# Kernel tuning notes

Hardware: AMD Instinct MI355X
Metric: run time of the kernel (lower is better)

The kernel has to match this reference:

```python
import jax, jax.numpy as jnp
import numpy as np

INPUT_SIZE = 128
HIDDEN = 256
EPS = 1e-5  # PyTorch BatchNorm1d default


def setup_inputs() -> dict:
    key = jax.random.key(0)
    k1, k2, k3 = jax.random.split(key, 3)
    B, S = 128, 1024
    x = jax.random.normal(k1, (B, S, INPUT_SIZE), dtype=jnp.float32)
    fan_in = INPUT_SIZE + HIDDEN
    bound = 1.0 / np.sqrt(fan_in)
    # Linear(input+hidden -> 4*hidden); stored transposed for x @ W
    W = jax.random.uniform(k2, (fan_in, 4 * HIDDEN), minval=-bound, maxval=bound, dtype=jnp.float32)
    b = jax.random.uniform(k3, (4 * HIDDEN,), minval=-bound, maxval=bound, dtype=jnp.float32)
    gamma = jnp.ones((4, HIDDEN), dtype=jnp.float32)   # per-gate BN weight
    beta = jnp.zeros((4, HIDDEN), dtype=jnp.float32)   # per-gate BN bias
    return {"x": x, "W": W, "b": b, "gamma": gamma, "beta": beta}


def reference(x, W, b, gamma, beta):
    B, S, _ = x.shape
    H = HIDDEN

    def step(carry, x_t):
        hx, cx = carry
        g = jnp.concatenate([x_t, hx], axis=1) @ W + b          # [B, 4H]
        g = g.reshape(B, 4, H)
        # BatchNorm1d (training mode): batch statistics per gate/feature
        mean = g.mean(axis=0)                                   # [4, H]
        var = jnp.mean((g - mean) ** 2, axis=0)                 # biased var
        gn = (g - mean) * jax.lax.rsqrt(var + EPS) * gamma + beta
        i = jax.nn.sigmoid(gn[:, 0])
        f = jax.nn.sigmoid(gn[:, 1])
        c = jnp.tanh(gn[:, 2])
        o = jax.nn.sigmoid(gn[:, 3])
        cy = f * cx + i * c
        hy = o * jnp.tanh(cy)
        return (hy, cy), hy

    h0 = jnp.zeros((B, H), dtype=x.dtype)
    c0 = jnp.zeros((B, H), dtype=x.dtype)
    (hy, cy), outs = jax.lax.scan(step, (h0, c0), jnp.swapaxes(x, 0, 1))
    outputs = jnp.swapaxes(outs, 0, 1)                          # [B, S, H]
    return outputs, hy, cy
```

## Files before the change

### kernel.cpp

```cpp
#include <hip/hip_runtime.h>

#define BATCH 128
#define SEQ   1024
#define INSZ  128
#define HID   256
#define NBLK  32
#define NTHR  512
#define FPB   8
#define EPSV  1e-5f

typedef __attribute__((ext_vector_type(4))) float f32x4;
typedef __attribute__((ext_vector_type(8))) short short8;
typedef __attribute__((ext_vector_type(4))) unsigned u32x4;
typedef unsigned u32;

__device__ __forceinline__ unsigned short f2bf(float f) {
  unsigned u = __builtin_bit_cast(unsigned, f);
  u += 0x7FFFu + ((u >> 16) & 1u);
  return (unsigned short)(u >> 16);
}
__device__ __forceinline__ short8 xcvt(float4 f0, float4 f1) {
  u32 a, b, c, d2;
  asm("v_cvt_pk_bf16_f32 %0, %1, %2" : "=v"(a)  : "v"(f0.x), "v"(f0.y));
  asm("v_cvt_pk_bf16_f32 %0, %1, %2" : "=v"(b)  : "v"(f0.z), "v"(f0.w));
  asm("v_cvt_pk_bf16_f32 %0, %1, %2" : "=v"(c)  : "v"(f1.x), "v"(f1.y));
  asm("v_cvt_pk_bf16_f32 %0, %1, %2" : "=v"(d2) : "v"(f1.z), "v"(f1.w));
  u32x4 t = {a, b, c, d2};
  return __builtin_bit_cast(short8, t);
}

__launch_bounds__(NTHR)
__global__ void bnlstm_kernel(const float* __restrict__ x,
                              const float* __restrict__ W,
                              const float* __restrict__ gamma,
                              const float* __restrict__ beta,
                              float* __restrict__ out,
                              unsigned short* __restrict__ hbuf,
                              u32* __restrict__ flags) {
  __shared__ __attribute__((aligned(16))) unsigned short Zs[32 * 1024];
  __shared__ float red1[2][8][32];
  __shared__ float red2[2][8][32];
  __shared__ float waveTr[8][16][17];
  __shared__ __attribute__((aligned(16))) unsigned short hpack[8][16][8];

  const int tid   = threadIdx.x;
  const int bid   = blockIdx.x;
  const int lane  = tid & 63;
  const int wid   = tid >> 6;
  const int col16 = lane & 15;
  const int kg    = lane >> 4;
  const int d     = col16 & 3;
  const int q     = col16 >> 2;
  const int arow  = wid * 16 + col16;
  const int brow  = wid * 16 + kg * 4 + d;

  short8 wf[2][12];
  for (int cg = 0; cg < 2; ++cg) {
    const int c32 = cg * 16 + col16;
    const int wcol = (c32 & 3) * HID + bid * FPB + (c32 >> 2);
    for (int kt = 0; kt < 12; ++kt) {
      short8 v;
      for (int e = 0; e < 8; ++e)
        v[e] = (short)f2bf(W[(kt * 32 + kg * 8 + e) * 1024 + wcol]);
      wf[cg][kt] = v;
    }
  }
  float gam = 0.f, bet = 0.f;
  if (lane < 32) {
    gam = gamma[(lane & 3) * HID + bid * FPB + (lane >> 2)];
    bet = beta [(lane & 3) * HID + bid * FPB + (lane >> 2)];
  }

  float cst[2] = {0.f, 0.f};
  float hnv[2];

  const float* xbase = x + (size_t)arow * (SEQ * INSZ) + kg * 8;
  float4 xv[8];
  #pragma unroll
  for (int kt = 0; kt < 4; ++kt) {
    xv[2 * kt]     = *(const float4*)(xbase + kt * 32);
    xv[2 * kt + 1] = *(const float4*)(xbase + kt * 32 + 4);
  }

  for (int t = 0; t < SEQ; ++t) {
    const int pR = t & 1;
    f32x4 acc0 = {0.f, 0.f, 0.f, 0.f}, acc1 = {0.f, 0.f, 0.f, 0.f};

    #pragma unroll
    for (int kt = 0; kt < 4; ++kt) {
      short8 ax = xcvt(xv[2 * kt], xv[2 * kt + 1]);
      acc0 = __builtin_amdgcn_mfma_f32_16x16x32_bf16(ax, wf[0][kt], acc0, 0, 0, 0);
      acc1 = __builtin_amdgcn_mfma_f32_16x16x32_bf16(ax, wf[1][kt], acc1, 0, 0, 0);
    }
    if (t + 1 < SEQ) {
      const float* xr = xbase + (size_t)(t + 1) * INSZ;
      #pragma unroll
      for (int kt = 0; kt < 4; ++kt) {
        xv[2 * kt]     = *(const float4*)(xr + kt * 32);
        xv[2 * kt + 1] = *(const float4*)(xr + kt * 32 + 4);
      }
    }

    if (t > 0) {
      {
        const u32 tv = (u32)t;
        while (true) {
          u32 v = (lane < NBLK)
            ? __hip_atomic_load(&flags[(lane * 8 + wid) * 32], __ATOMIC_RELAXED,
                                __HIP_MEMORY_SCOPE_AGENT)
            : tv;
          if (__all((int)(v >= tv))) break;
          __builtin_amdgcn_s_sleep(1);
        }
      }
      const unsigned short* hsrc = hbuf + pR * (BATCH * HID);
      u32x4 hvv[8];
      #pragma unroll
      for (int k = 0; k < 8; ++k) {
        const unsigned short* ap = hsrc + ((k * 4 + kg) * 128 + arow) * 8;
        asm volatile("global_load_dwordx4 %0, %1, off sc0 sc1"
                     : "=v"(hvv[k]) : "v"(ap));
      }
      asm volatile("s_waitcnt vmcnt(0)" ::: "memory");
      __builtin_amdgcn_sched_barrier(0);
      #pragma unroll
      for (int k = 0; k < 8; ++k)
        *(u32x4*)&Zs[((k * 4 + kg) * 128 + arow) * 8] = hvv[k];

      #pragma unroll
      for (int kt = 0; kt < 8; ++kt) {
        short8 af = *(const short8*)&Zs[((kt * 4 + kg) * 128 + arow) * 8];
        acc0 = __builtin_amdgcn_mfma_f32_16x16x32_bf16(af, wf[0][4 + kt], acc0, 0, 0, 0);
        acc1 = __builtin_amdgcn_mfma_f32_16x16x32_bf16(af, wf[1][4 + kt], acc1, 0, 0, 0);
      }
    }

    {
      float a1 = acc0[0] + acc0[1] + acc0[2] + acc0[3];
      float b1 = acc0[0]*acc0[0] + acc0[1]*acc0[1] + acc0[2]*acc0[2] + acc0[3]*acc0[3];
      float a2 = acc1[0] + acc1[1] + acc1[2] + acc1[3];
      float b2 = acc1[0]*acc1[0] + acc1[1]*acc1[1] + acc1[2]*acc1[2] + acc1[3]*acc1[3];
      a1 += __shfl_xor(a1, 16); b1 += __shfl_xor(b1, 16);
      a1 += __shfl_xor(a1, 32); b1 += __shfl_xor(b1, 32);
      a2 += __shfl_xor(a2, 16); b2 += __shfl_xor(b2, 16);
      a2 += __shfl_xor(a2, 32); b2 += __shfl_xor(b2, 32);
      if (lane < 16) {
        red1[pR][wid][lane] = a1;       red2[pR][wid][lane] = b1;
        red1[pR][wid][16 + lane] = a2;  red2[pR][wid][16 + lane] = b2;
      }
    }
    __syncthreads();

    float sc0v, sh0v, sc1v, sh1v;
    {
      const int cidx = lane & 31;
      float S1 = 0.f, S2 = 0.f;
      #pragma unroll
      for (int w2 = 0; w2 < 8; ++w2) { S1 += red1[pR][w2][cidx]; S2 += red2[pR][w2][cidx]; }
      float mean = S1 * (1.f / BATCH);
      float var  = fmaxf(S2 * (1.f / BATCH) - mean * mean, 0.f);
      float scl = rsqrtf(var + EPSV) * gam;
      float shl = bet - mean * scl;
      sc0v = __shfl(scl, col16);       sh0v = __shfl(shl, col16);
      sc1v = __shfl(scl, 16 + col16);  sh1v = __shfl(shl, 16 + col16);
    }

    #pragma unroll
    for (int cg = 0; cg < 2; ++cg) {
      f32x4 a = cg ? acc1 : acc0;
      const float sc = cg ? sc1v : sc0v, sh = cg ? sh1v : sh0v;
      #pragma unroll
      for (int i = 0; i < 4; ++i)
        waveTr[wid][kg * 4 + i][col16] = a[i] * sc + sh;
      float g0 = waveTr[wid][kg * 4 + d][q * 4 + 0];
      float g1 = waveTr[wid][kg * 4 + d][q * 4 + 1];
      float g2 = waveTr[wid][kg * 4 + d][q * 4 + 2];
      float g3 = waveTr[wid][kg * 4 + d][q * 4 + 3];
      float ig = __builtin_amdgcn_rcpf(1.f + __expf(-g0));
      float fg = __builtin_amdgcn_rcpf(1.f + __expf(-g1));
      float gg = 1.f - 2.f * __builtin_amdgcn_rcpf(__expf(2.f * g2) + 1.f);
      float og = __builtin_amdgcn_rcpf(1.f + __expf(-g3));
      float cn = fg * cst[cg] + ig * gg;
      float hn = og * (1.f - 2.f * __builtin_amdgcn_rcpf(__expf(2.f * cn) + 1.f));
      cst[cg] = cn;
      hnv[cg] = hn;
      hpack[wid][kg * 4 + d][cg * 4 + q] = f2bf(hn);
    }

    if (t < SEQ - 1) {
      if (lane < 16) {
        u32x4 hv = *(const u32x4*)&hpack[wid][lane][0];
        unsigned short* hd = hbuf + (pR ^ 1) * (BATCH * HID)
                           + (bid * 128 + wid * 16 + lane) * 8;
        asm volatile("global_store_dwordx4 %0, %1, off sc0 sc1"
                     :: "v"(hd), "v"(hv) : "memory");
      }
      asm volatile("s_waitcnt vmcnt(0)" ::: "memory");
      if (lane == 0)
        __hip_atomic_store(&flags[(bid * 8 + wid) * 32], (u32)(t + 1),
                           __ATOMIC_RELAXED, __HIP_MEMORY_SCOPE_AGENT);
      float* po = &out[(size_t)brow * (SEQ * HID) + (size_t)t * HID + bid * FPB];
      po[q]     = hnv[0];
      po[4 + q] = hnv[1];
    } else {
      float* po = &out[(size_t)brow * (SEQ * HID) + (size_t)t * HID + bid * FPB];
      po[q]     = hnv[0];
      po[4 + q] = hnv[1];
      float* ph = &out[(size_t)BATCH * SEQ * HID + (size_t)brow * HID + bid * FPB];
      ph[q] = hnv[0];                 ph[4 + q] = hnv[1];
      ph[BATCH * HID + q] = cst[0];   ph[BATCH * HID + 4 + q] = cst[1];
    }
  }
}

extern "C" void kernel_launch(void* const* d_in, const int* in_sizes, int n_in,
                              void* d_out, int out_size, void* d_ws, size_t ws_size,
                              hipStream_t stream) {
  const float* x     = (const float*)d_in[0];
  const float* W     = (const float*)d_in[1];
  const float* gamma = (const float*)d_in[3];
  const float* beta  = (const float*)d_in[4];
  float* out = (float*)d_out;

  u32* flags = (u32*)d_ws;
  unsigned short* hbuf = (unsigned short*)((char*)d_ws + 32768);

  (void)hipMemsetAsync(d_ws, 0, 32768, stream);
  hipLaunchKernelGGL(bnlstm_kernel, dim3(NBLK), dim3(NTHR), 0, stream,
                     x, W, gamma, beta, out, hbuf, flags);
}
```

Baseline: 4.623 ms.

## Replace flag-based inter-block sync with tag bits embedded in hidden-state data

```diff
diff --git a/kernel.cpp b/kernel.cpp
--- a/kernel.cpp
+++ b/kernel.cpp
@@ -35,8 +35,7 @@
                               const float* __restrict__ gamma,
                               const float* __restrict__ beta,
                               float* __restrict__ out,
-                              unsigned short* __restrict__ hbuf,
-                              u32* __restrict__ flags) {
+                              unsigned short* __restrict__ hbuf) {
   __shared__ __attribute__((aligned(16))) unsigned short Zs[32 * 1024];
   __shared__ float red1[2][8][32];
   __shared__ float red2[2][8][32];
@@ -102,26 +101,32 @@
     }
 
     if (t > 0) {
-      {
-        const u32 tv = (u32)t;
-        while (true) {
-          u32 v = (lane < NBLK)
-            ? __hip_atomic_load(&flags[(lane * 8 + wid) * 32], __ATOMIC_RELAXED,
-                                __HIP_MEMORY_SCOPE_AGENT)
-            : tv;
-          if (__all((int)(v >= tv))) break;
-          __builtin_amdgcn_s_sleep(1);
-        }
-      }
+      const u32 TB = ((u32)(t >> 1) & 0x7fu) | 0x80u;
+      const u32 e0 = ((TB >> 0) & 1u) | (((TB >> 1) & 1u) << 16);
+      const u32 e1 = ((TB >> 2) & 1u) | (((TB >> 3) & 1u) << 16);
+      const u32 e2 = ((TB >> 4) & 1u) | (((TB >> 5) & 1u) << 16);
+      const u32 e3 = ((TB >> 6) & 1u) | (((TB >> 7) & 1u) << 16);
       const unsigned short* hsrc = hbuf + pR * (BATCH * HID);
       u32x4 hvv[8];
-      #pragma unroll
-      for (int k = 0; k < 8; ++k) {
-        const unsigned short* ap = hsrc + ((k * 4 + kg) * 128 + arow) * 8;
-        asm volatile("global_load_dwordx4 %0, %1, off sc0 sc1"
-                     : "=v"(hvv[k]) : "v"(ap));
-      }
-      asm volatile("s_waitcnt vmcnt(0)" ::: "memory");
+      while (true) {
+        #pragma unroll
+        for (int k = 0; k < 8; ++k) {
+          const unsigned short* ap = hsrc + ((k * 4 + kg) * 128 + arow) * 8;
+          asm volatile("global_load_dwordx4 %0, %1, off sc0 sc1"
+                       : "=v"(hvv[k]) : "v"(ap));
+        }
+        asm volatile("s_waitcnt vmcnt(0)" ::: "memory");
+        u32 bad = 0;
+        #pragma unroll
+        for (int k = 0; k < 8; ++k) {
+          bad |= (hvv[k].x ^ e0) & 0x00010001u;
+          bad |= (hvv[k].y ^ e1) & 0x00010001u;
+          bad |= (hvv[k].z ^ e2) & 0x00010001u;
+          bad |= (hvv[k].w ^ e3) & 0x00010001u;
+        }
+        if (__all(bad == 0)) break;
+        __builtin_amdgcn_s_sleep(2);
+      }
       __builtin_amdgcn_sched_barrier(0);
       #pragma unroll
       for (int k = 0; k < 8; ++k)
@@ -165,6 +170,7 @@
       sc1v = __shfl(scl, 16 + col16);  sh1v = __shfl(shl, 16 + col16);
     }
 
+    const u32 TBn = ((u32)((t + 1) >> 1) & 0x7fu) | 0x80u;
     #pragma unroll
     for (int cg = 0; cg < 2; ++cg) {
       f32x4 a = cg ? acc1 : acc0;
@@ -184,7 +190,9 @@
       float hn = og * (1.f - 2.f * __builtin_amdgcn_rcpf(__expf(2.f * cn) + 1.f));
       cst[cg] = cn;
       hnv[cg] = hn;
-      hpack[wid][kg * 4 + d][cg * 4 + q] = f2bf(hn);
+      const int jl = cg * 4 + q;
+      hpack[wid][kg * 4 + d][jl] =
+          (unsigned short)((f2bf(hn) & 0xFFFEu) | ((TBn >> jl) & 1u));
     }
 
     if (t < SEQ - 1) {
@@ -195,10 +203,6 @@
         asm volatile("global_store_dwordx4 %0, %1, off sc0 sc1"
                      :: "v"(hd), "v"(hv) : "memory");
       }
-      asm volatile("s_waitcnt vmcnt(0)" ::: "memory");
-      if (lane == 0)
-        __hip_atomic_store(&flags[(bid * 8 + wid) * 32], (u32)(t + 1),
-                           __ATOMIC_RELAXED, __HIP_MEMORY_SCOPE_AGENT);
       float* po = &out[(size_t)brow * (SEQ * HID) + (size_t)t * HID + bid * FPB];
       po[q]     = hnv[0];
       po[4 + q] = hnv[1];
@@ -222,10 +226,9 @@
   const float* beta  = (const float*)d_in[4];
   float* out = (float*)d_out;
 
-  u32* flags = (u32*)d_ws;
-  unsigned short* hbuf = (unsigned short*)((char*)d_ws + 32768);
-
-  (void)hipMemsetAsync(d_ws, 0, 32768, stream);
+  unsigned short* hbuf = (unsigned short*)d_ws;
+
+  (void)hipMemsetAsync(d_ws, 0, 2 * BATCH * HID * sizeof(unsigned short), stream);
   hipLaunchKernelGGL(bnlstm_kernel, dim3(NBLK), dim3(NTHR), 0, stream,
-                     x, W, gamma, beta, out, hbuf, flags);
-}
+                     x, W, gamma, beta, out, hbuf);
+}
```

After: 4.676 ms. About the same (+1.1%).
